# Performance work log

Hardware: AMD Instinct MI355X
Metric: run time of the kernel (lower is better)

The kernel has to match this reference:

```python
import jax, jax.numpy as jnp
import numpy as np

B, T, D, H = 4, 2048, 1024, 16
DK = D // H  # 64


def setup_inputs() -> dict:
    key = jax.random.key(0)
    ks = jax.random.split(key, 7)
    s = 1.0 / np.sqrt(D)
    x = jax.random.normal(ks[0], (B, T, D), dtype=jnp.float32)
    W_qkv = jax.random.normal(ks[1], (D, 3 * D), dtype=jnp.float32) * s
    b_qkv = jnp.zeros((3 * D,), dtype=jnp.float32)
    W_out = jax.random.normal(ks[2], (D, D), dtype=jnp.float32) * s
    b_out = jnp.zeros((D,), dtype=jnp.float32)
    # rotary tables: standard inv-freq construction, shape [T, DK//2]
    inv_freq = 1.0 / (10000.0 ** (np.arange(0, DK, 2, dtype=np.float32) / DK))
    ang = jnp.asarray(np.arange(T, dtype=np.float32)[:, None] * inv_freq[None, :])
    cos = jnp.cos(ang)
    sin = jnp.sin(ang)
    return {"x": x, "W_qkv": W_qkv, "b_qkv": b_qkv, "W_out": W_out,
            "b_out": b_out, "cos": cos, "sin": sin}


def _rope(t, cos, sin):
    # t: [B, H, T, DK]; cos/sin: [T, DK//2] broadcast over B, H
    t1, t2 = t[..., ::2], t[..., 1::2]
    return jnp.concatenate([t1 * cos - t2 * sin, t1 * sin + t2 * cos], axis=-1)


def reference(x, W_qkv, b_qkv, W_out, b_out, cos, sin):
    Bx, Tx, C = x.shape
    dk = C // H
    qkv = (x @ W_qkv + b_qkv).reshape(Bx, Tx, H, 3 * dk).transpose(0, 2, 1, 3)
    q, k, v = jnp.split(qkv, 3, axis=-1)  # each [B, H, T, dk]
    q = _rope(q, cos, sin)
    k = _rope(k, cos, sin)
    scores = jnp.einsum("bhtd,bhsd->bhts", q, k) / jnp.sqrt(jnp.float32(dk))
    causal = jnp.tril(jnp.ones((Tx, Tx), dtype=bool))  # [T, T]
    scores = jnp.where(causal, scores, jnp.float32(-jnp.inf))
    w = jax.nn.softmax(scores, axis=-1)  # dropout p=0.0 (eval): identity
    attn = jnp.einsum("bhts,bhsd->bhtd", w, v)
    attn = attn.transpose(0, 2, 1, 3).reshape(Bx, Tx, C)
    return attn @ W_out + b_out
```

## Files before the change

kernel.cpp:

```cpp
#include <hip/hip_runtime.h>
#include <cmath>

typedef __attribute__((ext_vector_type(4))) float f32x4;
typedef __attribute__((ext_vector_type(16))) float f32x16;
typedef __attribute__((ext_vector_type(8))) __bf16 bf16x8;
typedef __attribute__((ext_vector_type(8))) short s16x8;
typedef __attribute__((ext_vector_type(2))) unsigned int u32x2;

#define CB 4
#define CT 2048
#define CD 1024
#define CH 16
#define CDK 64
#define CBT 8192
#define CBH 64

#define GLOAD_LDS16(g, l)                                              \
  __builtin_amdgcn_global_load_lds(                                    \
      (const __attribute__((address_space(1))) unsigned int*)(g),      \
      (__attribute__((address_space(3))) unsigned int*)(l), 16, 0, 0)

__device__ __forceinline__ unsigned short f2bf(float f) {
  union { float f; unsigned u; } x; x.f = f;
  unsigned r = x.u + 0x7fffu + ((x.u >> 16) & 1u);
  return (unsigned short)(r >> 16);
}
__device__ __forceinline__ float bf2f(unsigned short b) {
  union { unsigned u; float f; } x; x.u = ((unsigned)b) << 16;
  return x.f;
}
__device__ __forceinline__ f32x4 mfma16(bf16x8 a, bf16x8 b, f32x4 c) {
  return __builtin_amdgcn_mfma_f32_16x16x32_bf16(a, b, c, 0, 0, 0);
}
__device__ __forceinline__ f32x16 mfma32(bf16x8 a, bf16x8 b, f32x16 c) {
  return __builtin_amdgcn_mfma_f32_32x32x16_bf16(a, b, c, 0, 0, 0);
}
__device__ __forceinline__ unsigned cvtpk(float lo, float hi) {
  unsigned r;
  asm("v_cvt_pk_bf16_f32 %0, %1, %2" : "=v"(r) : "v"(lo), "v"(hi));
  return r;
}

__global__ void prep_inputs(const float* __restrict__ x,
                            unsigned short* __restrict__ xb,
                            const float* __restrict__ wqkv,
                            unsigned short* __restrict__ wqt,
                            const float* __restrict__ wout,
                            unsigned short* __restrict__ wot) {
  __shared__ float tile[32][33];
  const int b = blockIdx.x, tid = threadIdx.x;
  if (b < 8192) {
    const int i = (b * 256 + tid) * 4;
    float4 v = *(const float4*)(x + i);
    ushort4 o;
    o.x = f2bf(v.x); o.y = f2bf(v.y); o.z = f2bf(v.z); o.w = f2bf(v.w);
    *(ushort4*)(xb + i) = o;
    return;
  }
  const int bt = b - 8192;
  const int bx = bt & 127, rt = bt >> 7;
  const int xx = tid & 31, y0 = tid >> 5;
  const float* src;
  unsigned short* dst;
  int C, ct;
  if (bx < 96) { src = wqkv; dst = wqt; C = 3072; ct = bx; }
  else         { src = wout; dst = wot; C = 1024; ct = bx - 96; }
  const int R = 1024;
#pragma unroll
  for (int k = 0; k < 4; ++k) {
    int r = rt * 32 + y0 + k * 8;
    tile[y0 + k * 8][xx] = src[(size_t)r * C + ct * 32 + xx];
  }
  __syncthreads();
#pragma unroll
  for (int k = 0; k < 4; ++k) {
    int c = ct * 32 + y0 + k * 8;
    dst[(size_t)c * R + rt * 32 + xx] = f2bf(tile[xx][y0 + k * 8]);
  }
}

template <int MODE>
__global__ __launch_bounds__(256, 4) void gemm_bt(
    const unsigned short* __restrict__ A, const unsigned short* __restrict__ Bt,
    const float* __restrict__ bias, unsigned short* __restrict__ o0,
    unsigned short* __restrict__ o1, unsigned short* __restrict__ o2,
    float* __restrict__ fout, const float* __restrict__ cosT,
    const float* __restrict__ sinT, int M, int N, int K) {
  __shared__ __align__(16) unsigned short As[128 * 64];
  __shared__ __align__(16) unsigned short Bs[128 * 64];
  const int tid = threadIdx.x;
  const int lane = tid & 63, wid = tid >> 6;
  const int wr = wid >> 1, wc = wid & 1;
  const int m0 = blockIdx.x * 128, n0 = blockIdx.y * 128;
  const int l15 = lane & 15, l4 = lane >> 4;
  const int rx = l15 & 7;

  f32x4 acc[4][4];
#pragma unroll
  for (int i = 0; i < 4; ++i)
#pragma unroll
    for (int j = 0; j < 4; ++j) acc[i][j] = (f32x4){0.f, 0.f, 0.f, 0.f};

  const int srow = tid >> 3;
  const int scol = ((tid & 7) ^ (srow & 7)) * 8;
  const unsigned short* ag = A + (size_t)(m0 + srow) * K + scol;
  const unsigned short* bg = Bt + (size_t)(n0 + srow) * K + scol;
  unsigned short* asd = As + wid * 512;
  unsigned short* bsd = Bs + wid * 512;

  for (int k0 = 0; k0 < K; k0 += 64) {
#pragma unroll
    for (int p = 0; p < 4; ++p) {
      GLOAD_LDS16(ag + (size_t)(p * 32) * K + k0, asd + p * 2048);
      GLOAD_LDS16(bg + (size_t)(p * 32) * K + k0, bsd + p * 2048);
    }
    __syncthreads();
#pragma unroll
    for (int kk = 0; kk < 2; ++kk) {
      const int gsw = ((kk * 4 + l4) ^ rx) * 8;
      bf16x8 af[4], bfr[4];
#pragma unroll
      for (int i = 0; i < 4; ++i)
        af[i] = *(const bf16x8*)(&As[(wr * 64 + i * 16 + l15) * 64 + gsw]);
#pragma unroll
      for (int j = 0; j < 4; ++j)
        bfr[j] = *(const bf16x8*)(&Bs[(wc * 64 + j * 16 + l15) * 64 + gsw]);
#pragma unroll
      for (int i = 0; i < 4; ++i)
#pragma unroll
        for (int j = 0; j < 4; ++j)
          acc[i][j] = mfma16(af[i], bfr[j], acc[i][j]);
    }
    __syncthreads();
  }

  if (MODE == 1) {
#pragma unroll
    for (int i = 0; i < 4; ++i)
#pragma unroll
      for (int j = 0; j < 4; ++j) {
        const int row0 = m0 + wr * 64 + i * 16 + l4 * 4;
        const int col = n0 + wc * 64 + j * 16 + l15;
        const float bv = bias[col];
#pragma unroll
        for (int r = 0; r < 4; ++r)
          fout[(size_t)(row0 + r) * N + col] = acc[i][j][r] + bv;
      }
  } else {
#pragma unroll
    for (int i = 0; i < 4; ++i)
#pragma unroll
      for (int j = 0; j < 4; ++j) {
        const int col = n0 + wc * 64 + j * 16 + l15;
        const float bv = bias[col];
        const int h = col / 192;
        const int c = col % 192;
        const int sel = c >> 6;
        const int d = c & 63;
        if (sel < 2) {
          const int p = d >> 1;
          const float sgn = (d & 1) ? 1.0f : -1.0f;
          const float qsc = (sel == 0) ? 0.18033688011112042592f : 1.0f;
          unsigned short* dst = (sel == 0) ? o0 : o1;
#pragma unroll
          for (int r = 0; r < 4; ++r) {
            const int row = m0 + wr * 64 + i * 16 + l4 * 4 + r;
            const int b = row >> 11, t = row & 2047;
            const float v = acc[i][j][r] + bv;
            const float vp = __shfl_xor(v, 1);
            const float cs = cosT[t * 32 + p];
            const float sn = sinT[t * 32 + p];
            const float res = (v * cs + sgn * vp * sn) * qsc;
            dst[((size_t)((b * CH + h) * CT + t)) * CDK + d] = f2bf(res);
          }
        } else {
          const int t0g = m0 + wr * 64 + i * 16 + l4 * 4;
          const int b = t0g >> 11, t = t0g & 2047;
          ushort4 pk;
          pk.x = f2bf(acc[i][j][0] + bv);
          pk.y = f2bf(acc[i][j][1] + bv);
          pk.z = f2bf(acc[i][j][2] + bv);
          pk.w = f2bf(acc[i][j][3] + bv);
          *(ushort4*)(&o2[((size_t)((b * CH + h) * CDK + d)) * CT + t]) = pk;
        }
      }
  }
}

__global__ __launch_bounds__(512, 4) void attn_fwd6(
    const unsigned short* __restrict__ qg, const unsigned short* __restrict__ kg,
    const unsigned short* __restrict__ vtg, unsigned short* __restrict__ ctx) {
  __shared__ __align__(16) unsigned short smem[32768];
  unsigned short* Ks = smem;
  unsigned short* Vt = smem + 16384;
  const int tid = threadIdx.x, lane = tid & 63, w = tid >> 6;
  const int l31 = lane & 31, hi = lane >> 5;
  const int b1 = blockIdx.x;
  const int g8 = b1 & 7, idx8 = b1 >> 3;
  const int qb = 7 - (idx8 & 7);
  const int bh = g8 + 8 * (idx8 >> 3);
  const unsigned short* qp = qg + ((size_t)bh * CT + qb * 256) * CDK;
  const unsigned short* kp = kg + (size_t)bh * CT * CDK;
  const unsigned short* vp = vtg + (size_t)bh * CDK * CT;

  bf16x8 qf[4];
  {
    const unsigned short* qrow = qp + (size_t)(w * 32 + l31) * CDK + hi * 8;
#pragma unroll
    for (int ks = 0; ks < 4; ++ks) qf[ks] = *(const bf16x8*)(qrow + ks * 16);
  }
#pragma unroll
  for (int ks = 0; ks < 4; ++ks)
    asm volatile("" :: "v"(*(const f32x4*)&qf[ks]));

  const int lr = lane >> 3;
  const int srow = w * 8 + lr;
  const int gsw = ((lane & 7) ^ lr) * 8;
  const unsigned short* ksrc = kp + (size_t)srow * CDK + gsw;
  const unsigned short* vsrc = vp + (size_t)srow * CT + gsw;
  const int ldo = w * 512;

  const int NJ = 4 * qb + 4;
  const int njw = ((qb * 256 + w * 32 + 31) >> 6) + 1;
  const int qrow_g = qb * 256 + w * 32 + l31;

  auto STAGE = [&](int t) {
    const int buf = t & 3;
    GLOAD_LDS16(ksrc + (size_t)t * 64 * CDK, Ks + buf * 4096 + ldo);
    GLOAD_LDS16(vsrc + (size_t)t * 64, Vt + buf * 4096 + ldo);
  };

  f32x16 oacc[2];
#pragma unroll
  for (int nb = 0; nb < 2; ++nb)
#pragma unroll
    for (int r = 0; r < 16; ++r) oacc[nb][r] = 0.f;
  float lsum = 0.f;

  STAGE(0);
  STAGE(1);

  for (int j = 0; j < NJ; ++j) {
    if (j + 2 < NJ) STAGE(j + 2);
    const int pend = NJ - 1 - j;
    if (pend >= 2)      asm volatile("s_waitcnt vmcnt(4)" ::: "memory");
    else if (pend == 1) asm volatile("s_waitcnt vmcnt(2)" ::: "memory");
    else                asm volatile("s_waitcnt vmcnt(0)" ::: "memory");
    __builtin_amdgcn_s_barrier();

    if (j < njw) {
      const unsigned short* KB = Ks + (j & 3) * 4096;
      const unsigned short* VB = Vt + (j & 3) * 4096;

      f32x16 pacc[2];
      __builtin_amdgcn_s_setprio(1);
#pragma unroll
      for (int kb = 0; kb < 2; ++kb) {
#pragma unroll
        for (int r = 0; r < 16; ++r) pacc[kb][r] = 0.f;
#pragma unroll
        for (int ks = 0; ks < 4; ++ks) {
          const int row = kb * 32 + l31;
          bf16x8 kf = *(const bf16x8*)(KB + row * 64 + (((ks * 2 + hi) ^ (row & 7)) * 8));
          pacc[kb] = mfma32(kf, qf[ks], pacc[kb]);
        }
      }
      __builtin_amdgcn_s_setprio(0);

      if (j == njw - 1) {
        const int key0 = j * 64;
#pragma unroll
        for (int kb = 0; kb < 2; ++kb)
#pragma unroll
          for (int r = 0; r < 16; ++r) {
            const int key = key0 + kb * 32 + (r & 3) + 8 * (r >> 2) + 4 * hi;
            if (key > qrow_g) pacc[kb][r] = -1e30f;
          }
      }

#pragma unroll
      for (int kb = 0; kb < 2; ++kb)
#pragma unroll
        for (int r = 0; r < 16; ++r)
          pacc[kb][r] = __builtin_amdgcn_exp2f(pacc[kb][r]);
      float rs;
      {
        float t[16];
#pragma unroll
        for (int r = 0; r < 16; ++r) t[r] = pacc[0][r] + pacc[1][r];
#pragma unroll
        for (int s = 8; s > 0; s >>= 1)
#pragma unroll
          for (int r = 0; r < s; ++r) t[r] += t[r + s];
        rs = t[0];
      }
      {
        unsigned ru = __float_as_uint(rs);
        u32x2 sw = __builtin_amdgcn_permlane32_swap(ru, ru, false, false);
        rs += __uint_as_float(hi ? sw[0] : sw[1]);
      }
      lsum += rs;

      bf16x8 pf[4];
#pragma unroll
      for (int kb = 0; kb < 2; ++kb)
#pragma unroll
        for (int half = 0; half < 2; ++half) {
          const int b0i = half * 8;
          unsigned c0 = cvtpk(pacc[kb][b0i + 0], pacc[kb][b0i + 1]);
          unsigned c1 = cvtpk(pacc[kb][b0i + 2], pacc[kb][b0i + 3]);
          unsigned c2 = cvtpk(pacc[kb][b0i + 4], pacc[kb][b0i + 5]);
          unsigned c3 = cvtpk(pacc[kb][b0i + 6], pacc[kb][b0i + 7]);
          u32x2 r02 = __builtin_amdgcn_permlane32_swap(c0, c2, false, false);
          u32x2 r13 = __builtin_amdgcn_permlane32_swap(c1, c3, false, false);
          union { unsigned u[4]; bf16x8 v; } fr;
          fr.u[0] = r02[0]; fr.u[1] = r13[0]; fr.u[2] = r02[1]; fr.u[3] = r13[1];
          pf[kb * 2 + half] = fr.v;
        }

      __builtin_amdgcn_s_setprio(1);
#pragma unroll
      for (int nb = 0; nb < 2; ++nb)
#pragma unroll
        for (int ks = 0; ks < 4; ++ks) {
          const int row = nb * 32 + l31;
          bf16x8 vf = *(const bf16x8*)(VB + row * 64 + (((ks * 2 + hi) ^ (row & 7)) * 8));
          oacc[nb] = mfma32(vf, pf[ks], oacc[nb]);
        }
      __builtin_amdgcn_s_setprio(0);
    }
  }

  __syncthreads();

  unsigned short* tr = smem + w * 2048;
  const float inv = 1.f / lsum;
#pragma unroll
  for (int nb = 0; nb < 2; ++nb)
#pragma unroll
    for (int rp = 0; rp < 8; ++rp) {
      const int r = rp * 2;
      unsigned pkd = cvtpk(oacc[nb][r] * inv, oacc[nb][r + 1] * inv);
      const int d = nb * 32 + (r & 3) + 8 * (r >> 2) + 4 * hi;
      const int g = (d >> 3) ^ (l31 & 7);
      *(unsigned*)(tr + l31 * 64 + g * 8 + (d & 7)) = pkd;
    }
  const int b = bh >> 4, h = bh & 15;
#pragma unroll
  for (int s = 0; s < 4; ++s) {
    const int c = s * 64 + lane;
    const int qr = c >> 3, g = c & 7;
    s16x8 row = *(const s16x8*)(tr + qr * 64 + ((g ^ (qr & 7))) * 8);
    const int tok = qb * 256 + w * 32 + qr;
    *(s16x8*)(ctx + ((size_t)(b * CT + tok)) * CD + h * CDK + g * 8) = row;
  }
}

extern "C" void kernel_launch(void* const* d_in, const int* in_sizes, int n_in,
                              void* d_out, int out_size, void* d_ws, size_t ws_size,
                              hipStream_t stream) {
  (void)in_sizes; (void)n_in; (void)out_size; (void)ws_size;
  const float* x     = (const float*)d_in[0];
  const float* W_qkv = (const float*)d_in[1];
  const float* b_qkv = (const float*)d_in[2];
  const float* W_out = (const float*)d_in[3];
  const float* b_out = (const float*)d_in[4];
  const float* cosT  = (const float*)d_in[5];
  const float* sinT  = (const float*)d_in[6];
  float* out = (float*)d_out;

  unsigned short* xb   = (unsigned short*)d_ws;
  unsigned short* wqt  = xb + (size_t)CBT * CD;
  unsigned short* wot  = wqt + (size_t)3 * CD * CD;
  unsigned short* qbuf = wot + (size_t)CD * CD;
  unsigned short* kbuf = qbuf + (size_t)CBH * CT * CDK;
  unsigned short* vbuf = kbuf + (size_t)CBH * CT * CDK;
  unsigned short* ctx  = vbuf + (size_t)CBH * CT * CDK;

  prep_inputs<<<dim3(8192 + 4096), 256, 0, stream>>>(x, xb, W_qkv, wqt,
                                                     W_out, wot);
  gemm_bt<0><<<dim3(CBT / 128, 3 * CD / 128), 256, 0, stream>>>(
      xb, wqt, b_qkv, qbuf, kbuf, vbuf, nullptr, cosT, sinT, CBT, 3 * CD, CD);
  attn_fwd6<<<dim3(512), 512, 0, stream>>>(qbuf, kbuf, vbuf, ctx);
  gemm_bt<1><<<dim3(CBT / 128, CD / 128), 256, 0, stream>>>(
      ctx, wot, b_out, nullptr, nullptr, nullptr, out, nullptr, nullptr,
      CBT, CD, CD);
}
```

Baseline: 161.4 us.

## Split long causal query blocks across two workgroups with a separate reduce kernel

Splits the KV loop of the four longest causal query blocks (qb 4-7) into two halves, each handled by its own workgroup, so the grid grows from 512 to 768 workgroups with more even work per workgroup. Split workgroups write unnormalised fp32 partial outputs and row sums to workspace, and a new reduce kernel adds the halves, normalises, and writes bf16 context. The aim is to cut the tail imbalance of causal attention. In exchange it adds a kernel launch plus fp32 partial traffic to and from global memory. It also relies on a fixed softmax offset so the halves combine without max rescaling.

```diff
diff --git a/kernel.cpp b/kernel.cpp
--- a/kernel.cpp
+++ b/kernel.cpp
@@ -187,18 +187,26 @@
   }
 }
 
-__global__ __launch_bounds__(512, 4) void attn_fwd6(
+__global__ __launch_bounds__(512, 4) void attn_fwd7(
     const unsigned short* __restrict__ qg, const unsigned short* __restrict__ kg,
-    const unsigned short* __restrict__ vtg, unsigned short* __restrict__ ctx) {
+    const unsigned short* __restrict__ vtg, unsigned short* __restrict__ ctx,
+    float* __restrict__ opart, float* __restrict__ lpart) {
   __shared__ __align__(16) unsigned short smem[32768];
   unsigned short* Ks = smem;
   unsigned short* Vt = smem + 16384;
   const int tid = threadIdx.x, lane = tid & 63, w = tid >> 6;
   const int l31 = lane & 31, hi = lane >> 5;
-  const int b1 = blockIdx.x;
-  const int g8 = b1 & 7, idx8 = b1 >> 3;
-  const int qb = 7 - (idx8 & 7);
-  const int bh = g8 + 8 * (idx8 >> 3);
+  const int g8 = blockIdx.x & 7, r = blockIdx.x >> 3;
+  const int bh = g8 + 8 * (r / 12);
+  const int sub = r % 12;
+  const int qb = (int)((0x014455266773ULL >> (sub * 4)) & 15);
+  const int ch = (0x294 >> sub) & 1;
+  const int split = (0x3DE >> sub) & 1;
+  const int NJ = 4 * qb + 4;
+  const int halfn = 2 * qb + 2;
+  const int jbeg = ch * halfn;
+  const int jend = split ? (jbeg + halfn) : NJ;
+
   const unsigned short* qp = qg + ((size_t)bh * CT + qb * 256) * CDK;
   const unsigned short* kp = kg + (size_t)bh * CT * CDK;
   const unsigned short* vp = vtg + (size_t)bh * CDK * CT;
@@ -220,7 +228,6 @@
   const unsigned short* vsrc = vp + (size_t)srow * CT + gsw;
   const int ldo = w * 512;
 
-  const int NJ = 4 * qb + 4;
   const int njw = ((qb * 256 + w * 32 + 31) >> 6) + 1;
   const int qrow_g = qb * 256 + w * 32 + l31;
 
@@ -234,15 +241,15 @@
 #pragma unroll
   for (int nb = 0; nb < 2; ++nb)
 #pragma unroll
-    for (int r = 0; r < 16; ++r) oacc[nb][r] = 0.f;
+    for (int r2 = 0; r2 < 16; ++r2) oacc[nb][r2] = 0.f;
   float lsum = 0.f;
 
-  STAGE(0);
-  STAGE(1);
-
-  for (int j = 0; j < NJ; ++j) {
-    if (j + 2 < NJ) STAGE(j + 2);
-    const int pend = NJ - 1 - j;
+  STAGE(jbeg);
+  STAGE(jbeg + 1);
+
+  for (int j = jbeg; j < jend; ++j) {
+    if (j + 2 < jend) STAGE(j + 2);
+    const int pend = jend - 1 - j;
     if (pend >= 2)      asm volatile("s_waitcnt vmcnt(4)" ::: "memory");
     else if (pend == 1) asm volatile("s_waitcnt vmcnt(2)" ::: "memory");
     else                asm volatile("s_waitcnt vmcnt(0)" ::: "memory");
@@ -257,7 +264,7 @@
 #pragma unroll
       for (int kb = 0; kb < 2; ++kb) {
 #pragma unroll
-        for (int r = 0; r < 16; ++r) pacc[kb][r] = 0.f;
+        for (int r2 = 0; r2 < 16; ++r2) pacc[kb][r2] = 0.f;
 #pragma unroll
         for (int ks = 0; ks < 4; ++ks) {
           const int row = kb * 32 + l31;
@@ -272,26 +279,26 @@
 #pragma unroll
         for (int kb = 0; kb < 2; ++kb)
 #pragma unroll
-          for (int r = 0; r < 16; ++r) {
-            const int key = key0 + kb * 32 + (r & 3) + 8 * (r >> 2) + 4 * hi;
-            if (key > qrow_g) pacc[kb][r] = -1e30f;
+          for (int r2 = 0; r2 < 16; ++r2) {
+            const int key = key0 + kb * 32 + (r2 & 3) + 8 * (r2 >> 2) + 4 * hi;
+            if (key > qrow_g) pacc[kb][r2] = -1e30f;
           }
       }
 
 #pragma unroll
       for (int kb = 0; kb < 2; ++kb)
 #pragma unroll
-        for (int r = 0; r < 16; ++r)
-          pacc[kb][r] = __builtin_amdgcn_exp2f(pacc[kb][r]);
+        for (int r2 = 0; r2 < 16; ++r2)
+          pacc[kb][r2] = __builtin_amdgcn_exp2f(pacc[kb][r2]);
       float rs;
       {
         float t[16];
 #pragma unroll
-        for (int r = 0; r < 16; ++r) t[r] = pacc[0][r] + pacc[1][r];
+        for (int r2 = 0; r2 < 16; ++r2) t[r2] = pacc[0][r2] + pacc[1][r2];
 #pragma unroll
         for (int s = 8; s > 0; s >>= 1)
 #pragma unroll
-          for (int r = 0; r < s; ++r) t[r] += t[r + s];
+          for (int r2 = 0; r2 < s; ++r2) t[r2] += t[r2 + s];
         rs = t[0];
       }
       {
@@ -333,27 +340,66 @@
 
   __syncthreads();
 
-  unsigned short* tr = smem + w * 2048;
-  const float inv = 1.f / lsum;
-#pragma unroll
-  for (int nb = 0; nb < 2; ++nb)
-#pragma unroll
-    for (int rp = 0; rp < 8; ++rp) {
-      const int r = rp * 2;
-      unsigned pkd = cvtpk(oacc[nb][r] * inv, oacc[nb][r + 1] * inv);
-      const int d = nb * 32 + (r & 3) + 8 * (r >> 2) + 4 * hi;
-      const int g = (d >> 3) ^ (l31 & 7);
-      *(unsigned*)(tr + l31 * 64 + g * 8 + (d & 7)) = pkd;
+  if (!split) {
+    unsigned short* tr = smem + w * 2048;
+    const float inv = 1.f / lsum;
+#pragma unroll
+    for (int nb = 0; nb < 2; ++nb)
+#pragma unroll
+      for (int rp = 0; rp < 8; ++rp) {
+        const int r2 = rp * 2;
+        unsigned pkd = cvtpk(oacc[nb][r2] * inv, oacc[nb][r2 + 1] * inv);
+        const int d = nb * 32 + (r2 & 3) + 8 * (r2 >> 2) + 4 * hi;
+        const int g = (d >> 3) ^ (l31 & 7);
+        *(unsigned*)(tr + l31 * 64 + g * 8 + (d & 7)) = pkd;
+      }
+    const int b = bh >> 4, h = bh & 15;
+#pragma unroll
+    for (int s = 0; s < 4; ++s) {
+      const int c = s * 64 + lane;
+      const int qr = c >> 3, g = c & 7;
+      s16x8 row = *(const s16x8*)(tr + qr * 64 + ((g ^ (qr & 7))) * 8);
+      const int tok = qb * 256 + w * 32 + qr;
+      *(s16x8*)(ctx + ((size_t)(b * CT + tok)) * CD + h * CDK + g * 8) = row;
     }
+  } else {
+    float* trw = (float*)smem + w * 2048;
+#pragma unroll
+    for (int nb = 0; nb < 2; ++nb)
+#pragma unroll
+      for (int r2 = 0; r2 < 16; ++r2) {
+        const int d = nb * 32 + (r2 & 3) + 8 * (r2 >> 2) + 4 * hi;
+        trw[l31 * 64 + (((d >> 2) ^ (l31 & 15)) << 2) + (d & 3)] = oacc[nb][r2];
+      }
+    const int tokrel0 = qb * 256 + w * 32 - 1024;
+    const size_t pbase = (size_t)(ch * 65536 + bh * 1024 + tokrel0);
+#pragma unroll
+    for (int s = 0; s < 8; ++s) {
+      const int idx = s * 64 + lane;
+      const int row = idx >> 4, gq = idx & 15;
+      f32x4 v = *(const f32x4*)(trw + row * 64 + (((gq ^ (row & 15)) << 2)));
+      *(f32x4*)(opart + (pbase + row) * 64 + gq * 4) = v;
+    }
+    if (hi == 0) lpart[ch * 65536 + bh * 1024 + tokrel0 + l31] = lsum;
+  }
+}
+
+__global__ __launch_bounds__(256) void attn_reduce(
+    const float* __restrict__ opart, const float* __restrict__ lpart,
+    unsigned short* __restrict__ ctx) {
+  const int gid = blockIdx.x * 256 + threadIdx.x;
+  const int row = gid >> 4, dq = (gid & 15) << 2;
+  f32x4 a = *(const f32x4*)(opart + (size_t)row * 64 + dq);
+  f32x4 b4 = *(const f32x4*)(opart + ((size_t)65536 + row) * 64 + dq);
+  const float inv = 1.f / (lpart[row] + lpart[65536 + row]);
+  ushort4 o;
+  o.x = f2bf((a[0] + b4[0]) * inv);
+  o.y = f2bf((a[1] + b4[1]) * inv);
+  o.z = f2bf((a[2] + b4[2]) * inv);
+  o.w = f2bf((a[3] + b4[3]) * inv);
+  const int bh = row >> 10, tokrel = row & 1023;
   const int b = bh >> 4, h = bh & 15;
-#pragma unroll
-  for (int s = 0; s < 4; ++s) {
-    const int c = s * 64 + lane;
-    const int qr = c >> 3, g = c & 7;
-    s16x8 row = *(const s16x8*)(tr + qr * 64 + ((g ^ (qr & 7))) * 8);
-    const int tok = qb * 256 + w * 32 + qr;
-    *(s16x8*)(ctx + ((size_t)(b * CT + tok)) * CD + h * CDK + g * 8) = row;
-  }
+  *(ushort4*)(ctx + ((size_t)(b * CT + 1024 + tokrel)) * CD + h * CDK + dq) = o;
 }
 
 extern "C" void kernel_launch(void* const* d_in, const int* in_sizes, int n_in,
@@ -376,12 +422,15 @@
   unsigned short* kbuf = qbuf + (size_t)CBH * CT * CDK;
   unsigned short* vbuf = kbuf + (size_t)CBH * CT * CDK;
   unsigned short* ctx  = vbuf + (size_t)CBH * CT * CDK;
+  float* opart = (float*)(ctx + (size_t)CBT * CD);
+  float* lpart = opart + (size_t)2 * 65536 * 64;
 
   prep_inputs<<<dim3(8192 + 4096), 256, 0, stream>>>(x, xb, W_qkv, wqt,
                                                      W_out, wot);
   gemm_bt<0><<<dim3(CBT / 128, 3 * CD / 128), 256, 0, stream>>>(
       xb, wqt, b_qkv, qbuf, kbuf, vbuf, nullptr, cosT, sinT, CBT, 3 * CD, CD);
-  attn_fwd6<<<dim3(512), 512, 0, stream>>>(qbuf, kbuf, vbuf, ctx);
+  attn_fwd7<<<dim3(768), 512, 0, stream>>>(qbuf, kbuf, vbuf, ctx, opart, lpart);
+  attn_reduce<<<dim3(4096), 256, 0, stream>>>(opart, lpart, ctx);
   gemm_bt<1><<<dim3(CBT / 128, CD / 128), 256, 0, stream>>>(
       ctx, wot, b_out, nullptr, nullptr, nullptr, out, nullptr, nullptr,
       CBT, CD, CD);
```

Result: no change. 161.2 us (median of 2 runs) (-0.1%).
